# Performance work log

Hardware: AMD Instinct MI355X
Metric: run time of the kernel (lower is better)

The kernel has to match this reference:

```python
import jax, jax.numpy as jnp
import numpy as np

H = 4            # num_heads (forced: 128 projection / d_k=32)
DK = 32          # hardcoded d_k
SCALE = 1.0 / np.sqrt(32.0)
EPS = 1e-5       # LayerNorm eps (torch default)


def setup_inputs() -> dict:
    key = jax.random.key(0)
    ks = jax.random.split(key, 8)
    B, L, Dq, Dkv, M = 16, 4096, 512, 512, 512
    def w(k, shape, fan_in):
        return (jax.random.normal(k, shape, jnp.float32) / np.sqrt(fan_in)).astype(jnp.float32)
    return {
        "Q_in":  jax.random.normal(ks[0], (B, L, Dq),  jnp.float32),
        "KV_in": jax.random.normal(ks[1], (B, L, Dkv), jnp.float32),
        "Wq":  w(ks[2], (Dq, 128), Dq),   "bq":  jnp.zeros((128,), jnp.float32),
        "Wk":  w(ks[3], (Dkv, 128), Dkv), "bk":  jnp.zeros((128,), jnp.float32),
        "Wv":  w(ks[4], (Dkv, 128), Dkv), "bv":  jnp.zeros((128,), jnp.float32),
        "Wo":  w(ks[5], (128, M), 128),   "bo":  jnp.zeros((M,), jnp.float32),
        "Wqo": w(ks[6], (128, M), 128),   "bqo": jnp.zeros((M,), jnp.float32),
        "gamma": jnp.ones((M,), jnp.float32),
        "beta":  jnp.zeros((M,), jnp.float32),
    }


def reference(Q_in, KV_in, Wq, bq, Wk, bk, Wv, bv, Wo, bo, Wqo, bqo, gamma, beta):
    B, L, _ = Q_in.shape
    Qm = Q_in @ Wq + bq          # (B, L, 128)
    Km = KV_in @ Wk + bk         # (B, L, 128)
    Vm = KV_in @ Wv + bv         # (B, L, 128)

    def heads(X):
        # view(B, L, H, DK).permute(0, 2, 3, 1) -> (B, H, DK, L)
        return X.reshape(B, L, H, DK).transpose(0, 2, 3, 1)

    Qh, Kh, Vh = heads(Qm), heads(Km), heads(Vm)
    # matmul contracts over the SEQUENCE dim -> feature-feature scores (B,H,DK,DK)
    scores = jnp.einsum('bhdl,bhel->bhde', Qh, Kh) * SCALE
    attn = jax.nn.softmax(scores, axis=-1)          # dropout = identity (eval)
    out_h = jnp.einsum('bhde,bhel->bhdl', attn, Vh)  # (B, H, DK, L)
    out_h = out_h.transpose(0, 3, 1, 2).reshape(B, L, H * DK)  # (B, L, 128)

    out = out_h @ Wo + bo        # (B, L, M)
    Qm_ = Qm @ Wqo + bqo         # (B, L, M)
    x = Qm_ + out
    mu = jnp.mean(x, axis=-1, keepdims=True)
    var = jnp.var(x, axis=-1, keepdims=True)
    y = (x - mu) * jax.lax.rsqrt(var + EPS) * gamma + beta
    return (y, attn)
```

## Files before the change

### kernel.cpp

```cpp
#include <hip/hip_runtime.h>
#include <hip/hip_bf16.h>

typedef __bf16   bf16x8 __attribute__((ext_vector_type(8)));
typedef _Float16 f16x8  __attribute__((ext_vector_type(8)));
typedef float    f32x4  __attribute__((ext_vector_type(4)));

#define SCALE_QK 0.17677669529663687f
#define LDSS 40
#define TL   136

__device__ __forceinline__ float b2f(ushort u) {
    __hip_bfloat16 h; *reinterpret_cast<ushort*>(&h) = u; return __bfloat162float(h);
}
__device__ __forceinline__ ushort f2b(float f) {
    __hip_bfloat16 h = __float2bfloat16(f); return *reinterpret_cast<ushort*>(&h);
}
__device__ __forceinline__ ushort f2h(float f) {
    union { _Float16 h; ushort u; } x; x.h = (_Float16)f; return x.u;
}
__device__ __forceinline__ uint4 cvt8(float4 a, float4 b) {
    union { uint4 v; ushort u[8]; } H;
    H.u[0] = f2h(a.x); H.u[1] = f2h(a.y); H.u[2] = f2h(a.z); H.u[3] = f2h(a.w);
    H.u[4] = f2h(b.x); H.u[5] = f2h(b.y); H.u[6] = f2h(b.z); H.u[7] = f2h(b.w);
    return H.v;
}

__global__ void k_prep(const float* __restrict__ Wq, const float* __restrict__ Wk,
                       const float* __restrict__ Wv, const float* __restrict__ Wqo,
                       const float* __restrict__ Wo,
                       ushort* __restrict__ WqT, ushort* __restrict__ WkT,
                       ushort* __restrict__ WvT, ushort* __restrict__ WqoT,
                       ushort* __restrict__ WoB) {
    int idx = blockIdx.x * 256 + threadIdx.x;
    int mat = idx >> 16, i = idx & 65535;
    if (mat == 0) {
        int n = i >> 9, k = i & 511;
        WqT[i] = f2h(Wq[k * 128 + n]);
    } else if (mat == 1) {
        int n = i >> 9, k = i & 511;
        WkT[i] = f2h(Wk[k * 128 + n]);
    } else if (mat == 2) {
        int n = i >> 9, k = i & 511;
        WvT[i] = f2h(Wv[k * 128 + n]);
    } else if (mat == 3) {
        int n = i >> 7, k = i & 127;
        WqoT[i] = f2b(Wqo[k * 512 + n]);
    } else if (mat == 4) {
        WoB[i] = f2b(Wo[i]);
    }
}

__global__ __launch_bounds__(256) void k_qkv_scores(
        const float* __restrict__ Qin, const float* __restrict__ KVin,
        const ushort* __restrict__ WqT, const ushort* __restrict__ WkT,
        const ushort* __restrict__ WvT,
        const float* __restrict__ bq, const float* __restrict__ bk,
        const float* __restrict__ bv,
        ushort* __restrict__ QmB, ushort* __restrict__ VmB,
        float* __restrict__ partial) {
    __shared__ __align__(16) ushort lds[2 * 128 * TL];
    ushort* P1  = lds;
    ushort* P2  = lds + 128 * TL;
    ushort* As  = P2;
    ushort* Bs0 = P2 + 128 * LDSS;
    ushort* Bs1 = P2 + 2 * 128 * LDSS;

    const int row0 = blockIdx.x * 128;
    const int tid  = threadIdx.x;
    const int wid  = tid >> 6, lane = tid & 63;
    const int wm = wid >> 1, wn = wid & 1;
    const int quad = lane >> 4, l16 = lane & 15;
    const int sr = tid >> 2;
    const int sc = (tid & 3) * 8;

    float4 aR0, aR1, aR2, aR3;
    uint4  bR0, bR1;
    uint4  cR0, cR1;

    {
        f32x4 acc[4][4] = {};
        {
            const float* Ab = Qin + (size_t)(row0 + sr) * 512 + sc;
            aR0 = *(const float4*)Ab;
            aR1 = *(const float4*)(Ab + 4);
            aR2 = *(const float4*)(Ab + (size_t)64 * 512);
            aR3 = *(const float4*)(Ab + (size_t)64 * 512 + 4);
            bR0 = *(const uint4*)&WqT[(size_t)sr * 512 + sc];
            bR1 = *(const uint4*)&WqT[(size_t)(sr + 64) * 512 + sc];
        }
        for (int k0 = 0; k0 < 512; k0 += 32) {
            __syncthreads();
            *(uint4*)&As[sr * LDSS + sc]        = cvt8(aR0, aR1);
            *(uint4*)&As[(sr + 64) * LDSS + sc] = cvt8(aR2, aR3);
            *(uint4*)&Bs0[sr * LDSS + sc]        = bR0;
            *(uint4*)&Bs0[(sr + 64) * LDSS + sc] = bR1;
            if (k0 < 480) {
                const float* Ab = Qin + (size_t)(row0 + sr) * 512 + k0 + 32 + sc;
                aR0 = *(const float4*)Ab;
                aR1 = *(const float4*)(Ab + 4);
                aR2 = *(const float4*)(Ab + (size_t)64 * 512);
                aR3 = *(const float4*)(Ab + (size_t)64 * 512 + 4);
                bR0 = *(const uint4*)&WqT[(size_t)sr * 512 + k0 + 32 + sc];
                bR1 = *(const uint4*)&WqT[(size_t)(sr + 64) * 512 + k0 + 32 + sc];
            }
            __syncthreads();
            f16x8 aF[4];
#pragma unroll
            for (int i = 0; i < 4; ++i)
                aF[i] = *reinterpret_cast<const f16x8*>(&As[(wm * 64 + i * 16 + l16) * LDSS + quad * 8]);
#pragma unroll
            for (int j = 0; j < 4; ++j) {
                f16x8 bF = *reinterpret_cast<const f16x8*>(&Bs0[(wn * 64 + j * 16 + l16) * LDSS + quad * 8]);
#pragma unroll
                for (int i = 0; i < 4; ++i)
                    acc[i][j] = __builtin_amdgcn_mfma_f32_16x16x32_f16(aF[i], bF, acc[i][j], 0, 0, 0);
            }
        }
        {
            const float* Ab = KVin + (size_t)(row0 + sr) * 512 + sc;
            aR0 = *(const float4*)Ab;
            aR1 = *(const float4*)(Ab + 4);
            aR2 = *(const float4*)(Ab + (size_t)64 * 512);
            aR3 = *(const float4*)(Ab + (size_t)64 * 512 + 4);
            bR0 = *(const uint4*)&WkT[(size_t)sr * 512 + sc];
            bR1 = *(const uint4*)&WkT[(size_t)(sr + 64) * 512 + sc];
            cR0 = *(const uint4*)&WvT[(size_t)sr * 512 + sc];
            cR1 = *(const uint4*)&WvT[(size_t)(sr + 64) * 512 + sc];
        }
#pragma unroll
        for (int j = 0; j < 4; ++j) {
            int col = wn * 64 + j * 16 + l16;
            float bqv = bq[col];
#pragma unroll
            for (int i = 0; i < 4; ++i)
#pragma unroll
                for (int r = 0; r < 4; ++r) {
                    int row = wm * 64 + i * 16 + quad * 4 + r;
                    float v = acc[i][j][r] + bqv;
                    QmB[(size_t)(row0 + row) * 128 + col] = f2b(v);
                    P1[col * TL + row] = f2h(v);
                }
        }
    }

    {
        f32x4 accK[4][4] = {};
        f32x4 accV[4][4] = {};
        for (int k0 = 0; k0 < 512; k0 += 32) {
            __syncthreads();
            *(uint4*)&As[sr * LDSS + sc]        = cvt8(aR0, aR1);
            *(uint4*)&As[(sr + 64) * LDSS + sc] = cvt8(aR2, aR3);
            *(uint4*)&Bs0[sr * LDSS + sc]        = bR0;
            *(uint4*)&Bs0[(sr + 64) * LDSS + sc] = bR1;
            *(uint4*)&Bs1[sr * LDSS + sc]        = cR0;
            *(uint4*)&Bs1[(sr + 64) * LDSS + sc] = cR1;
            if (k0 < 480) {
                const float* Ab = KVin + (size_t)(row0 + sr) * 512 + k0 + 32 + sc;
                aR0 = *(const float4*)Ab;
                aR1 = *(const float4*)(Ab + 4);
                aR2 = *(const float4*)(Ab + (size_t)64 * 512);
                aR3 = *(const float4*)(Ab + (size_t)64 * 512 + 4);
                bR0 = *(const uint4*)&WkT[(size_t)sr * 512 + k0 + 32 + sc];
                bR1 = *(const uint4*)&WkT[(size_t)(sr + 64) * 512 + k0 + 32 + sc];
                cR0 = *(const uint4*)&WvT[(size_t)sr * 512 + k0 + 32 + sc];
                cR1 = *(const uint4*)&WvT[(size_t)(sr + 64) * 512 + k0 + 32 + sc];
            }
            __syncthreads();
            f16x8 aF[4];
#pragma unroll
            for (int i = 0; i < 4; ++i)
                aF[i] = *reinterpret_cast<const f16x8*>(&As[(wm * 64 + i * 16 + l16) * LDSS + quad * 8]);
#pragma unroll
            for (int j = 0; j < 4; ++j) {
                f16x8 bK = *reinterpret_cast<const f16x8*>(&Bs0[(wn * 64 + j * 16 + l16) * LDSS + quad * 8]);
                f16x8 bV = *reinterpret_cast<const f16x8*>(&Bs1[(wn * 64 + j * 16 + l16) * LDSS + quad * 8]);
#pragma unroll
                for (int i = 0; i < 4; ++i) {
                    accK[i][j] = __builtin_amdgcn_mfma_f32_16x16x32_f16(aF[i], bK, accK[i][j], 0, 0, 0);
                    accV[i][j] = __builtin_amdgcn_mfma_f32_16x16x32_f16(aF[i], bV, accV[i][j], 0, 0, 0);
                }
            }
        }
        __syncthreads();
#pragma unroll
        for (int j = 0; j < 4; ++j) {
            int col = wn * 64 + j * 16 + l16;
            float bkv = bk[col], bvv = bv[col];
#pragma unroll
            for (int i = 0; i < 4; ++i)
#pragma unroll
                for (int r = 0; r < 4; ++r) {
                    int row = wm * 64 + i * 16 + quad * 4 + r;
                    float vv = accV[i][j][r] + bvv;
                    VmB[(size_t)(row0 + row) * 128 + col] = f2b(vv);
                    P2[col * TL + row] = f2h(accK[i][j][r] + bkv);
                }
        }
    }
    __syncthreads();

    {
        const int h = wid;
        f32x4 s[2][2] = {};
#pragma unroll
        for (int ks = 0; ks < 4; ++ks) {
            f16x8 qa[2], kb[2];
#pragma unroll
            for (int dt = 0; dt < 2; ++dt)
                qa[dt] = *reinterpret_cast<const f16x8*>(
                    &P1[(h * 32 + dt * 16 + l16) * TL + ks * 32 + quad * 8]);
#pragma unroll
            for (int et = 0; et < 2; ++et)
                kb[et] = *reinterpret_cast<const f16x8*>(
                    &P2[(h * 32 + et * 16 + l16) * TL + ks * 32 + quad * 8]);
#pragma unroll
            for (int dt = 0; dt < 2; ++dt)
#pragma unroll
                for (int et = 0; et < 2; ++et)
                    s[dt][et] = __builtin_amdgcn_mfma_f32_16x16x32_f16(qa[dt], kb[et], s[dt][et], 0, 0, 0);
        }
        const int b = blockIdx.x >> 5, sp = blockIdx.x & 31;
        float* P = partial + (size_t)(sp * 64 + b * 4 + h) * 1024;
#pragma unroll
        for (int dt = 0; dt < 2; ++dt)
#pragma unroll
            for (int et = 0; et < 2; ++et)
#pragma unroll
                for (int r = 0; r < 4; ++r) {
                    int d = dt * 16 + quad * 4 + r, e = et * 16 + l16;
                    P[d * 32 + e] = s[dt][et][r];
                }
    }
}

__global__ __launch_bounds__(256) void k_attn(
        const float* __restrict__ partial, const ushort* __restrict__ WoB,
        float* __restrict__ attnOut, ushort* __restrict__ WcT) {
    int bh = blockIdx.x; int b = bh >> 2, h = bh & 3;
    __shared__ float aS[1024];
    __shared__ __align__(16) ushort wS[32 * 512];
    int t = threadIdx.x;
    for (int i = t; i < 1024; i += 256) {
        float s = 0.f;
#pragma unroll
        for (int sp = 0; sp < 32; ++sp)
            s += partial[(size_t)(sp * 64 + bh) * 1024 + i];
        aS[i] = s * SCALE_QK;
    }
    for (int i = t; i < 2048; i += 256) {
        int r = i >> 6, c = (i & 63) * 8;
        *(uint4*)&wS[r * 512 + c] = *(const uint4*)&WoB[(size_t)(h * 32 + r) * 512 + c];
    }
    __syncthreads();
    if (t < 32) {
        float m = -1e30f;
#pragma unroll
        for (int e = 0; e < 32; ++e) m = fmaxf(m, aS[t * 32 + e]);
        float p[32]; float sum = 0.f;
#pragma unroll
        for (int e = 0; e < 32; ++e) { p[e] = __expf(aS[t * 32 + e] - m); sum += p[e]; }
        float inv = 1.f / sum;
#pragma unroll
        for (int e = 0; e < 32; ++e) aS[t * 32 + e] = p[e] * inv;
    }
    __syncthreads();
    for (int i = t; i < 1024; i += 256)
        attnOut[(size_t)bh * 1024 + i] = aS[i];
    int e = t & 31, mg = t >> 5;
    for (int mi = 0; mi < 64; ++mi) {
        int m = mg * 64 + mi;
        float acc = 0.f;
#pragma unroll
        for (int d = 0; d < 32; ++d)
            acc += aS[d * 32 + e] * b2f(wS[d * 512 + m]);
        WcT[((size_t)b * 512 + m) * 128 + h * 32 + e] = f2b(acc);
    }
}

__global__ __launch_bounds__(256) void k_out_ln(
        const ushort* __restrict__ Vm, const ushort* __restrict__ Qm,
        const ushort* __restrict__ WcT, const ushort* __restrict__ WqoT,
        const float* __restrict__ bo, const float* __restrict__ bqo,
        const float* __restrict__ gamma, const float* __restrict__ beta,
        float* __restrict__ Y) {
    __shared__ __align__(16) ushort As[64 * LDSS];
    __shared__ __align__(16) ushort Bs[512 * LDSS];
    __shared__ float sumS[4][64], sumSS[4][64], muA[64], rsA[64];
    const int row0 = blockIdx.x * 64;
    const int b = row0 >> 12;
    const ushort* WcTb = WcT + (size_t)b * 512 * 128;
    const int tid = threadIdx.x;
    const int wid = tid >> 6, lane = tid & 63;
    const int quad = lane >> 4, l16 = lane & 15;
    const int sr = tid >> 2;
    const int sc = (tid & 3) * 8;

    f32x4 acc[4][8] = {};
    uint4 aR; uint4 bR[8];

    auto issueOL = [&](int k0) {
        const ushort* Asrc; const ushort* Bsrc; int kk;
        if (k0 < 128) { Asrc = Vm; Bsrc = WcTb; kk = k0; }
        else          { Asrc = Qm; Bsrc = WqoT; kk = k0 - 128; }
        aR = *(const uint4*)&Asrc[(size_t)(row0 + sr) * 128 + kk + sc];
#pragma unroll
        for (int p = 0; p < 8; ++p)
            bR[p] = *(const uint4*)&Bsrc[(size_t)(sr + p * 64) * 128 + kk + sc];
    };

    issueOL(0);
    for (int k0 = 0; k0 < 256; k0 += 32) {
        __syncthreads();
        *(uint4*)&As[sr * LDSS + sc] = aR;
#pragma unroll
        for (int p = 0; p < 8; ++p)
            *(uint4*)&Bs[(sr + p * 64) * LDSS + sc] = bR[p];
        if (k0 < 224) issueOL(k0 + 32);
        __syncthreads();
        bf16x8 aF[4];
#pragma unroll
        for (int i = 0; i < 4; ++i)
            aF[i] = *reinterpret_cast<const bf16x8*>(&As[(i * 16 + l16) * LDSS + quad * 8]);
#pragma unroll
        for (int j = 0; j < 8; ++j) {
            bf16x8 bF = *reinterpret_cast<const bf16x8*>(
                &Bs[(wid * 128 + j * 16 + l16) * LDSS + quad * 8]);
#pragma unroll
            for (int i = 0; i < 4; ++i)
                acc[i][j] = __builtin_amdgcn_mfma_f32_16x16x32_bf16(aF[i], bF, acc[i][j], 0, 0, 0);
        }
    }

    float bv[8];
#pragma unroll
    for (int j = 0; j < 8; ++j) {
        int ncol = wid * 128 + j * 16 + l16;
        bv[j] = bo[ncol] + bqo[ncol];
    }
    float sArr[4][4], ssArr[4][4];
#pragma unroll
    for (int i = 0; i < 4; ++i)
#pragma unroll
        for (int r = 0; r < 4; ++r) {
            float s = 0.f, ss = 0.f;
#pragma unroll
            for (int j = 0; j < 8; ++j) {
                float x = acc[i][j][r] + bv[j];
                s += x; ss += x * x;
            }
            sArr[i][r] = s; ssArr[i][r] = ss;
        }
#pragma unroll
    for (int off = 1; off < 16; off <<= 1)
#pragma unroll
        for (int i = 0; i < 4; ++i)
#pragma unroll
            for (int r = 0; r < 4; ++r) {
                sArr[i][r]  += __shfl_xor(sArr[i][r],  off, 64);
                ssArr[i][r] += __shfl_xor(ssArr[i][r], off, 64);
            }
    if (l16 == 0) {
#pragma unroll
        for (int i = 0; i < 4; ++i)
#pragma unroll
            for (int r = 0; r < 4; ++r) {
                int row = i * 16 + quad * 4 + r;
                sumS[wid][row]  = sArr[i][r];
                sumSS[wid][row] = ssArr[i][r];
            }
    }
    __syncthreads();
    if (tid < 64) {
        float s = sumS[0][tid] + sumS[1][tid] + sumS[2][tid] + sumS[3][tid];
        float ss = sumSS[0][tid] + sumSS[1][tid] + sumSS[2][tid] + sumSS[3][tid];
        float mu = s * (1.f / 512.f);
        float var = ss * (1.f / 512.f) - mu * mu;
        muA[tid] = mu;
        rsA[tid] = rsqrtf(var + 1e-5f);
    }
    __syncthreads();

    float gj[8], bj[8];
#pragma unroll
    for (int j = 0; j < 8; ++j) {
        int ncol = wid * 128 + j * 16 + l16;
        gj[j] = gamma[ncol]; bj[j] = beta[ncol];
    }
#pragma unroll
    for (int i = 0; i < 4; ++i)
#pragma unroll
        for (int r = 0; r < 4; ++r) {
            int row = i * 16 + quad * 4 + r;
            float mu = muA[row], rstd = rsA[row];
            size_t base = (size_t)(row0 + row) * 512 + wid * 128 + l16;
#pragma unroll
            for (int j = 0; j < 8; ++j) {
                float x = acc[i][j][r] + bv[j];
                Y[base + j * 16] = (x - mu) * rstd * gj[j] + bj[j];
            }
        }
}

extern "C" void kernel_launch(void* const* d_in, const int* in_sizes, int n_in,
                              void* d_out, int out_size, void* d_ws, size_t ws_size,
                              hipStream_t stream) {
    const float* Qin   = (const float*)d_in[0];
    const float* KVin  = (const float*)d_in[1];
    const float* Wq    = (const float*)d_in[2];
    const float* bq    = (const float*)d_in[3];
    const float* Wk    = (const float*)d_in[4];
    const float* bk    = (const float*)d_in[5];
    const float* Wv    = (const float*)d_in[6];
    const float* bv    = (const float*)d_in[7];
    const float* Wo    = (const float*)d_in[8];
    const float* bo    = (const float*)d_in[9];
    const float* Wqo   = (const float*)d_in[10];
    const float* bqo   = (const float*)d_in[11];
    const float* gamma = (const float*)d_in[12];
    const float* beta  = (const float*)d_in[13];
    float* out = (float*)d_out;
    float* attnOut = out + 33554432;

    char* ws = (char*)d_ws;
    ushort* WqT  = (ushort*)(ws);
    ushort* WkT  = (ushort*)(ws + 131072);
    ushort* WvT  = (ushort*)(ws + 262144);
    ushort* WqoT = (ushort*)(ws + 393216);
    ushort* WoB  = (ushort*)(ws + 524288);
    ushort* QmB  = (ushort*)(ws + 655360);
    ushort* VmB  = (ushort*)(ws + 17432576);
    float*  part = (float*) (ws + 34209792);
    ushort* WcT  = (ushort*)(ws + 42598400);

    k_prep<<<1280, 256, 0, stream>>>(Wq, Wk, Wv, Wqo, Wo,
                                     WqT, WkT, WvT, WqoT, WoB);
    k_qkv_scores<<<512, 256, 0, stream>>>(Qin, KVin, WqT, WkT, WvT,
                                          bq, bk, bv, QmB, VmB, part);
    k_attn<<<64, 256, 0, stream>>>(part, WoB, attnOut, WcT);
    k_out_ln<<<1024, 256, 0, stream>>>(VmB, QmB, WcT, WqoT, bo, bqo, gamma, beta, out);
}
```

Baseline: 472.6 us.

## Split QKV projection from score computation, parallelize k_attn across M tiles

The fused QKV+scores kernel is split in two. The projection kernel now writes fp16 Qm and Km to global memory and uses a smaller LDS footprint, and a new k_scores2 kernel reloads those tiles into swizzled LDS to compute the per-head feature-feature partial scores. k_attn is spread over a 2D grid of four M-quarters, uses a shuffle-based parallel softmax, and keeps Wo in fp32 LDS with the attention column held in registers. Register prefetching is removed from k_out_ln. The aim is higher occupancy and parallelism, paid for with extra global traffic for QmH/KmH, an extra launch, and redundant softmax work across the M-quarters.

```diff
diff --git a/kernel.cpp b/kernel.cpp
--- a/kernel.cpp
+++ b/kernel.cpp
@@ -7,7 +7,7 @@
 
 #define SCALE_QK 0.17677669529663687f
 #define LDSS 40
-#define TL   136
+#define RS   136
 
 __device__ __forceinline__ float b2f(ushort u) {
     __hip_bfloat16 h; *reinterpret_cast<ushort*>(&h) = u; return __bfloat162float(h);
@@ -50,20 +50,17 @@
     }
 }
 
-__global__ __launch_bounds__(256) void k_qkv_scores(
+__global__ __launch_bounds__(256) void k_qkv(
         const float* __restrict__ Qin, const float* __restrict__ KVin,
         const ushort* __restrict__ WqT, const ushort* __restrict__ WkT,
         const ushort* __restrict__ WvT,
         const float* __restrict__ bq, const float* __restrict__ bk,
         const float* __restrict__ bv,
-        ushort* __restrict__ QmB, ushort* __restrict__ VmB,
-        float* __restrict__ partial) {
-    __shared__ __align__(16) ushort lds[2 * 128 * TL];
-    ushort* P1  = lds;
-    ushort* P2  = lds + 128 * TL;
-    ushort* As  = P2;
-    ushort* Bs0 = P2 + 128 * LDSS;
-    ushort* Bs1 = P2 + 2 * 128 * LDSS;
+        ushort* __restrict__ QmB, ushort* __restrict__ QmH,
+        ushort* __restrict__ KmH, ushort* __restrict__ VmB) {
+    __shared__ __align__(16) ushort As [128 * LDSS];
+    __shared__ __align__(16) ushort Bs0[128 * LDSS];
+    __shared__ __align__(16) ushort Bs1[128 * LDSS];
 
     const int row0 = blockIdx.x * 128;
     const int tid  = threadIdx.x;
@@ -138,7 +135,7 @@
                     int row = wm * 64 + i * 16 + quad * 4 + r;
                     float v = acc[i][j][r] + bqv;
                     QmB[(size_t)(row0 + row) * 128 + col] = f2b(v);
-                    P1[col * TL + row] = f2h(v);
+                    QmH[(size_t)(row0 + row) * 128 + col] = f2h(v);
                 }
         }
     }
@@ -181,7 +178,6 @@
                 }
             }
         }
-        __syncthreads();
 #pragma unroll
         for (int j = 0; j < 4; ++j) {
             int col = wn * 64 + j * 16 + l16;
@@ -191,54 +187,77 @@
 #pragma unroll
                 for (int r = 0; r < 4; ++r) {
                     int row = wm * 64 + i * 16 + quad * 4 + r;
-                    float vv = accV[i][j][r] + bvv;
-                    VmB[(size_t)(row0 + row) * 128 + col] = f2b(vv);
-                    P2[col * TL + row] = f2h(accK[i][j][r] + bkv);
+                    KmH[(size_t)(row0 + row) * 128 + col] = f2h(accK[i][j][r] + bkv);
+                    VmB[(size_t)(row0 + row) * 128 + col] = f2b(accV[i][j][r] + bvv);
                 }
         }
     }
+}
+
+__global__ __launch_bounds__(256) void k_scores2(
+        const ushort* __restrict__ QmH, const ushort* __restrict__ KmH,
+        float* __restrict__ partial) {
+    __shared__ __align__(16) ushort Qs[128 * RS];
+    __shared__ __align__(16) ushort Ks[128 * RS];
+    const int bs = blockIdx.x;
+    const int b = bs >> 5, sp = bs & 31;
+    const int t = threadIdx.x;
+    const int wid = t >> 6, lane = t & 63;
+    const int quad = lane >> 4, l16 = lane & 15;
+    const size_t base = ((size_t)b * 4096 + sp * 128) * 128;
+
+#pragma unroll
+    for (int it = 0; it < 8; ++it) {
+        int idx = it * 256 + t;
+        int row = idx >> 4, c8 = (idx & 15) * 8;
+        int swc = c8 ^ (((row >> 3) & 3) << 3);
+        *(uint4*)&Qs[row * RS + swc] = *(const uint4*)&QmH[base + (size_t)row * 128 + c8];
+        *(uint4*)&Ks[row * RS + swc] = *(const uint4*)&KmH[base + (size_t)row * 128 + c8];
+    }
     __syncthreads();
 
-    {
-        const int h = wid;
-        f32x4 s[2][2] = {};
-#pragma unroll
-        for (int ks = 0; ks < 4; ++ks) {
-            f16x8 qa[2], kb[2];
-#pragma unroll
-            for (int dt = 0; dt < 2; ++dt)
-                qa[dt] = *reinterpret_cast<const f16x8*>(
-                    &P1[(h * 32 + dt * 16 + l16) * TL + ks * 32 + quad * 8]);
+    const int h = wid;
+    f32x4 s[2][2] = {};
+#pragma unroll
+    for (int ks = 0; ks < 4; ++ks) {
+        f16x8 qa[2], kb[2];
+#pragma unroll
+        for (int dt = 0; dt < 2; ++dt) {
+            union { f16x8 v; ushort u[8]; } Q, K;
+#pragma unroll
+            for (int z = 0; z < 8; ++z) {
+                int row = ks * 32 + quad * 8 + z;
+                int col = (h * 32 + dt * 16 + l16) ^ (((row >> 3) & 3) << 3);
+                Q.u[z] = Qs[row * RS + col];
+                K.u[z] = Ks[row * RS + col];
+            }
+            qa[dt] = Q.v; kb[dt] = K.v;
+        }
+#pragma unroll
+        for (int dt = 0; dt < 2; ++dt)
 #pragma unroll
             for (int et = 0; et < 2; ++et)
-                kb[et] = *reinterpret_cast<const f16x8*>(
-                    &P2[(h * 32 + et * 16 + l16) * TL + ks * 32 + quad * 8]);
-#pragma unroll
-            for (int dt = 0; dt < 2; ++dt)
-#pragma unroll
-                for (int et = 0; et < 2; ++et)
-                    s[dt][et] = __builtin_amdgcn_mfma_f32_16x16x32_f16(qa[dt], kb[et], s[dt][et], 0, 0, 0);
-        }
-        const int b = blockIdx.x >> 5, sp = blockIdx.x & 31;
-        float* P = partial + (size_t)(sp * 64 + b * 4 + h) * 1024;
-#pragma unroll
-        for (int dt = 0; dt < 2; ++dt)
-#pragma unroll
-            for (int et = 0; et < 2; ++et)
-#pragma unroll
-                for (int r = 0; r < 4; ++r) {
-                    int d = dt * 16 + quad * 4 + r, e = et * 16 + l16;
-                    P[d * 32 + e] = s[dt][et][r];
-                }
-    }
+                s[dt][et] = __builtin_amdgcn_mfma_f32_16x16x32_f16(qa[dt], kb[et], s[dt][et], 0, 0, 0);
+    }
+    float* P = partial + (size_t)(sp * 64 + b * 4 + h) * 1024;
+#pragma unroll
+    for (int dt = 0; dt < 2; ++dt)
+#pragma unroll
+        for (int et = 0; et < 2; ++et)
+#pragma unroll
+            for (int r = 0; r < 4; ++r) {
+                int d = dt * 16 + quad * 4 + r, e = et * 16 + l16;
+                P[d * 32 + e] = s[dt][et][r];
+            }
 }
 
 __global__ __launch_bounds__(256) void k_attn(
         const float* __restrict__ partial, const ushort* __restrict__ WoB,
         float* __restrict__ attnOut, ushort* __restrict__ WcT) {
     int bh = blockIdx.x; int b = bh >> 2, h = bh & 3;
+    int mq = blockIdx.y;
     __shared__ float aS[1024];
-    __shared__ __align__(16) ushort wS[32 * 512];
+    __shared__ float wSf[32 * 128];
     int t = threadIdx.x;
     for (int i = t; i < 1024; i += 256) {
         float s = 0.f;
@@ -247,32 +266,46 @@
             s += partial[(size_t)(sp * 64 + bh) * 1024 + i];
         aS[i] = s * SCALE_QK;
     }
-    for (int i = t; i < 2048; i += 256) {
-        int r = i >> 6, c = (i & 63) * 8;
-        *(uint4*)&wS[r * 512 + c] = *(const uint4*)&WoB[(size_t)(h * 32 + r) * 512 + c];
+    for (int i = t; i < 4096; i += 256) {
+        int r = i >> 7, c = i & 127;
+        wSf[i] = b2f(WoB[(size_t)(h * 32 + r) * 512 + mq * 128 + c]);
     }
     __syncthreads();
-    if (t < 32) {
-        float m = -1e30f;
-#pragma unroll
-        for (int e = 0; e < 32; ++e) m = fmaxf(m, aS[t * 32 + e]);
-        float p[32]; float sum = 0.f;
-#pragma unroll
-        for (int e = 0; e < 32; ++e) { p[e] = __expf(aS[t * 32 + e] - m); sum += p[e]; }
-        float inv = 1.f / sum;
-#pragma unroll
-        for (int e = 0; e < 32; ++e) aS[t * 32 + e] = p[e] * inv;
+    {
+        int row = t >> 3, sub = t & 7;
+        float v[4];
+#pragma unroll
+        for (int z = 0; z < 4; ++z) v[z] = aS[row * 32 + sub * 4 + z];
+        float m = fmaxf(fmaxf(v[0], v[1]), fmaxf(v[2], v[3]));
+#pragma unroll
+        for (int off = 1; off < 8; off <<= 1)
+            m = fmaxf(m, __shfl_xor(m, off, 64));
+        float pz[4], s = 0.f;
+#pragma unroll
+        for (int z = 0; z < 4; ++z) { pz[z] = __expf(v[z] - m); s += pz[z]; }
+#pragma unroll
+        for (int off = 1; off < 8; off <<= 1)
+            s += __shfl_xor(s, off, 64);
+        float inv = 1.f / s;
+#pragma unroll
+        for (int z = 0; z < 4; ++z) aS[row * 32 + sub * 4 + z] = pz[z] * inv;
     }
     __syncthreads();
-    for (int i = t; i < 1024; i += 256)
-        attnOut[(size_t)bh * 1024 + i] = aS[i];
+    if (mq == 0)
+        for (int i = t; i < 1024; i += 256)
+            attnOut[(size_t)bh * 1024 + i] = aS[i];
     int e = t & 31, mg = t >> 5;
-    for (int mi = 0; mi < 64; ++mi) {
-        int m = mg * 64 + mi;
+    float prow[32];
+#pragma unroll
+    for (int d = 0; d < 32; ++d) prow[d] = aS[d * 32 + e];
+#pragma unroll 4
+    for (int mi = 0; mi < 16; ++mi) {
+        int ml = mg * 16 + mi;
         float acc = 0.f;
 #pragma unroll
         for (int d = 0; d < 32; ++d)
-            acc += aS[d * 32 + e] * b2f(wS[d * 512 + m]);
+            acc += prow[d] * wSf[d * 128 + ml];
+        int m = mq * 128 + ml;
         WcT[((size_t)b * 512 + m) * 128 + h * 32 + e] = f2b(acc);
     }
 }
@@ -296,26 +329,19 @@
     const int sc = (tid & 3) * 8;
 
     f32x4 acc[4][8] = {};
-    uint4 aR; uint4 bR[8];
-
-    auto issueOL = [&](int k0) {
+
+    for (int k0 = 0; k0 < 256; k0 += 32) {
         const ushort* Asrc; const ushort* Bsrc; int kk;
         if (k0 < 128) { Asrc = Vm; Bsrc = WcTb; kk = k0; }
         else          { Asrc = Qm; Bsrc = WqoT; kk = k0 - 128; }
-        aR = *(const uint4*)&Asrc[(size_t)(row0 + sr) * 128 + kk + sc];
-#pragma unroll
-        for (int p = 0; p < 8; ++p)
-            bR[p] = *(const uint4*)&Bsrc[(size_t)(sr + p * 64) * 128 + kk + sc];
-    };
-
-    issueOL(0);
-    for (int k0 = 0; k0 < 256; k0 += 32) {
         __syncthreads();
-        *(uint4*)&As[sr * LDSS + sc] = aR;
-#pragma unroll
-        for (int p = 0; p < 8; ++p)
-            *(uint4*)&Bs[(sr + p * 64) * LDSS + sc] = bR[p];
-        if (k0 < 224) issueOL(k0 + 32);
+        *(uint4*)&As[sr * LDSS + sc] =
+            *(const uint4*)&Asrc[(size_t)(row0 + sr) * 128 + kk + sc];
+#pragma unroll
+        for (int p = 0; p < 8; ++p) {
+            int r = sr + p * 64;
+            *(uint4*)&Bs[r * LDSS + sc] = *(const uint4*)&Bsrc[(size_t)r * 128 + kk + sc];
+        }
         __syncthreads();
         bf16x8 aF[4];
 #pragma unroll
@@ -428,14 +454,17 @@
     ushort* WqoT = (ushort*)(ws + 393216);
     ushort* WoB  = (ushort*)(ws + 524288);
     ushort* QmB  = (ushort*)(ws + 655360);
-    ushort* VmB  = (ushort*)(ws + 17432576);
-    float*  part = (float*) (ws + 34209792);
-    ushort* WcT  = (ushort*)(ws + 42598400);
+    ushort* QmH  = (ushort*)(ws + 17432576);
+    ushort* KmH  = (ushort*)(ws + 34209792);
+    ushort* VmB  = (ushort*)(ws + 50987008);
+    float*  part = (float*) (ws + 67764224);
+    ushort* WcT  = (ushort*)(ws + 76152832);
 
     k_prep<<<1280, 256, 0, stream>>>(Wq, Wk, Wv, Wqo, Wo,
                                      WqT, WkT, WvT, WqoT, WoB);
-    k_qkv_scores<<<512, 256, 0, stream>>>(Qin, KVin, WqT, WkT, WvT,
-                                          bq, bk, bv, QmB, VmB, part);
-    k_attn<<<64, 256, 0, stream>>>(part, WoB, attnOut, WcT);
+    k_qkv<<<512, 256, 0, stream>>>(Qin, KVin, WqT, WkT, WvT,
+                                   bq, bk, bv, QmB, QmH, KmH, VmB);
+    k_scores2<<<512, 256, 0, stream>>>(QmH, KmH, part);
+    k_attn<<<dim3(64, 4), 256, 0, stream>>>(part, WoB, attnOut, WcT);
     k_out_ln<<<1024, 256, 0, stream>>>(VmB, QmB, WcT, WqoT, bo, bqo, gamma, beta, out);
 }
```

After: 436.5 us. -7.6%, faster.

## Switch intermediates to fp16, split k_attn over output columns, parallelize softmax

Applied to the files above, without the earlier changes.

Stores Qm, Vm, Wo, Wqo and the combined Wc intermediates as fp16 instead of bf16 and uses the f16 MFMA in the output/LayerNorm kernel. This lets the Q projection write one converted value to both global memory and LDS. k_attn now launches a 4x wider grid split over output columns, so 256 blocks share the Wo-combination work instead of 64. It also computes the softmax with all 256 threads using shuffles rather than 32 threads. The register prefetch in k_out_ln is removed, trading load/compute overlap for lower register pressure, and fp16 has a narrower dynamic range than bf16.

```diff
diff --git a/kernel.cpp b/kernel.cpp
--- a/kernel.cpp
+++ b/kernel.cpp
@@ -17,6 +17,9 @@
 }
 __device__ __forceinline__ ushort f2h(float f) {
     union { _Float16 h; ushort u; } x; x.h = (_Float16)f; return x.u;
+}
+__device__ __forceinline__ float h2f(ushort u) {
+    union { _Float16 h; ushort u; } x; x.u = u; return (float)x.h;
 }
 __device__ __forceinline__ uint4 cvt8(float4 a, float4 b) {
     union { uint4 v; ushort u[8]; } H;
@@ -30,7 +33,7 @@
                        const float* __restrict__ Wo,
                        ushort* __restrict__ WqT, ushort* __restrict__ WkT,
                        ushort* __restrict__ WvT, ushort* __restrict__ WqoT,
-                       ushort* __restrict__ WoB) {
+                       ushort* __restrict__ WoH) {
     int idx = blockIdx.x * 256 + threadIdx.x;
     int mat = idx >> 16, i = idx & 65535;
     if (mat == 0) {
@@ -44,9 +47,9 @@
         WvT[i] = f2h(Wv[k * 128 + n]);
     } else if (mat == 3) {
         int n = i >> 7, k = i & 127;
-        WqoT[i] = f2b(Wqo[k * 512 + n]);
+        WqoT[i] = f2h(Wqo[k * 512 + n]);
     } else if (mat == 4) {
-        WoB[i] = f2b(Wo[i]);
+        WoH[i] = f2h(Wo[i]);
     }
 }
 
@@ -56,7 +59,7 @@
         const ushort* __restrict__ WvT,
         const float* __restrict__ bq, const float* __restrict__ bk,
         const float* __restrict__ bv,
-        ushort* __restrict__ QmB, ushort* __restrict__ VmB,
+        ushort* __restrict__ QmH, ushort* __restrict__ VmH,
         float* __restrict__ partial) {
     __shared__ __align__(16) ushort lds[2 * 128 * TL];
     ushort* P1  = lds;
@@ -137,8 +140,9 @@
                 for (int r = 0; r < 4; ++r) {
                     int row = wm * 64 + i * 16 + quad * 4 + r;
                     float v = acc[i][j][r] + bqv;
-                    QmB[(size_t)(row0 + row) * 128 + col] = f2b(v);
-                    P1[col * TL + row] = f2h(v);
+                    ushort hv = f2h(v);
+                    QmH[(size_t)(row0 + row) * 128 + col] = hv;
+                    P1[col * TL + row] = hv;
                 }
         }
     }
@@ -191,8 +195,7 @@
 #pragma unroll
                 for (int r = 0; r < 4; ++r) {
                     int row = wm * 64 + i * 16 + quad * 4 + r;
-                    float vv = accV[i][j][r] + bvv;
-                    VmB[(size_t)(row0 + row) * 128 + col] = f2b(vv);
+                    VmH[(size_t)(row0 + row) * 128 + col] = f2h(accV[i][j][r] + bvv);
                     P2[col * TL + row] = f2h(accK[i][j][r] + bkv);
                 }
         }
@@ -234,11 +237,12 @@
 }
 
 __global__ __launch_bounds__(256) void k_attn(
-        const float* __restrict__ partial, const ushort* __restrict__ WoB,
+        const float* __restrict__ partial, const ushort* __restrict__ WoH,
         float* __restrict__ attnOut, ushort* __restrict__ WcT) {
     int bh = blockIdx.x; int b = bh >> 2, h = bh & 3;
+    int mq = blockIdx.y;
     __shared__ float aS[1024];
-    __shared__ __align__(16) ushort wS[32 * 512];
+    __shared__ float wSf[32 * 128];
     int t = threadIdx.x;
     for (int i = t; i < 1024; i += 256) {
         float s = 0.f;
@@ -247,33 +251,47 @@
             s += partial[(size_t)(sp * 64 + bh) * 1024 + i];
         aS[i] = s * SCALE_QK;
     }
-    for (int i = t; i < 2048; i += 256) {
-        int r = i >> 6, c = (i & 63) * 8;
-        *(uint4*)&wS[r * 512 + c] = *(const uint4*)&WoB[(size_t)(h * 32 + r) * 512 + c];
+    for (int i = t; i < 4096; i += 256) {
+        int r = i >> 7, c = i & 127;
+        wSf[i] = h2f(WoH[(size_t)(h * 32 + r) * 512 + mq * 128 + c]);
     }
     __syncthreads();
-    if (t < 32) {
-        float m = -1e30f;
-#pragma unroll
-        for (int e = 0; e < 32; ++e) m = fmaxf(m, aS[t * 32 + e]);
-        float p[32]; float sum = 0.f;
-#pragma unroll
-        for (int e = 0; e < 32; ++e) { p[e] = __expf(aS[t * 32 + e] - m); sum += p[e]; }
-        float inv = 1.f / sum;
-#pragma unroll
-        for (int e = 0; e < 32; ++e) aS[t * 32 + e] = p[e] * inv;
+    {
+        int row = t >> 3, sub = t & 7;
+        float v[4];
+#pragma unroll
+        for (int z = 0; z < 4; ++z) v[z] = aS[row * 32 + sub * 4 + z];
+        float m = fmaxf(fmaxf(v[0], v[1]), fmaxf(v[2], v[3]));
+#pragma unroll
+        for (int off = 1; off < 8; off <<= 1)
+            m = fmaxf(m, __shfl_xor(m, off, 64));
+        float pz[4], s = 0.f;
+#pragma unroll
+        for (int z = 0; z < 4; ++z) { pz[z] = __expf(v[z] - m); s += pz[z]; }
+#pragma unroll
+        for (int off = 1; off < 8; off <<= 1)
+            s += __shfl_xor(s, off, 64);
+        float inv = 1.f / s;
+#pragma unroll
+        for (int z = 0; z < 4; ++z) aS[row * 32 + sub * 4 + z] = pz[z] * inv;
     }
     __syncthreads();
-    for (int i = t; i < 1024; i += 256)
-        attnOut[(size_t)bh * 1024 + i] = aS[i];
+    if (mq == 0)
+        for (int i = t; i < 1024; i += 256)
+            attnOut[(size_t)bh * 1024 + i] = aS[i];
     int e = t & 31, mg = t >> 5;
-    for (int mi = 0; mi < 64; ++mi) {
-        int m = mg * 64 + mi;
+    float prow[32];
+#pragma unroll
+    for (int d = 0; d < 32; ++d) prow[d] = aS[d * 32 + e];
+#pragma unroll 4
+    for (int mi = 0; mi < 16; ++mi) {
+        int ml = mg * 16 + mi;
         float acc = 0.f;
 #pragma unroll
         for (int d = 0; d < 32; ++d)
-            acc += aS[d * 32 + e] * b2f(wS[d * 512 + m]);
-        WcT[((size_t)b * 512 + m) * 128 + h * 32 + e] = f2b(acc);
+            acc += prow[d] * wSf[d * 128 + ml];
+        int m = mq * 128 + ml;
+        WcT[((size_t)b * 512 + m) * 128 + h * 32 + e] = f2h(acc);
     }
 }
 
@@ -296,38 +314,31 @@
     const int sc = (tid & 3) * 8;
 
     f32x4 acc[4][8] = {};
-    uint4 aR; uint4 bR[8];
-
-    auto issueOL = [&](int k0) {
+
+    for (int k0 = 0; k0 < 256; k0 += 32) {
         const ushort* Asrc; const ushort* Bsrc; int kk;
         if (k0 < 128) { Asrc = Vm; Bsrc = WcTb; kk = k0; }
         else          { Asrc = Qm; Bsrc = WqoT; kk = k0 - 128; }
-        aR = *(const uint4*)&Asrc[(size_t)(row0 + sr) * 128 + kk + sc];
-#pragma unroll
-        for (int p = 0; p < 8; ++p)
-            bR[p] = *(const uint4*)&Bsrc[(size_t)(sr + p * 64) * 128 + kk + sc];
-    };
-
-    issueOL(0);
-    for (int k0 = 0; k0 < 256; k0 += 32) {
         __syncthreads();
-        *(uint4*)&As[sr * LDSS + sc] = aR;
-#pragma unroll
-        for (int p = 0; p < 8; ++p)
-            *(uint4*)&Bs[(sr + p * 64) * LDSS + sc] = bR[p];
-        if (k0 < 224) issueOL(k0 + 32);
+        *(uint4*)&As[sr * LDSS + sc] =
+            *(const uint4*)&Asrc[(size_t)(row0 + sr) * 128 + kk + sc];
+#pragma unroll
+        for (int p = 0; p < 8; ++p) {
+            int r = sr + p * 64;
+            *(uint4*)&Bs[r * LDSS + sc] = *(const uint4*)&Bsrc[(size_t)r * 128 + kk + sc];
+        }
         __syncthreads();
-        bf16x8 aF[4];
+        f16x8 aF[4];
 #pragma unroll
         for (int i = 0; i < 4; ++i)
-            aF[i] = *reinterpret_cast<const bf16x8*>(&As[(i * 16 + l16) * LDSS + quad * 8]);
+            aF[i] = *reinterpret_cast<const f16x8*>(&As[(i * 16 + l16) * LDSS + quad * 8]);
 #pragma unroll
         for (int j = 0; j < 8; ++j) {
-            bf16x8 bF = *reinterpret_cast<const bf16x8*>(
+            f16x8 bF = *reinterpret_cast<const f16x8*>(
                 &Bs[(wid * 128 + j * 16 + l16) * LDSS + quad * 8]);
 #pragma unroll
             for (int i = 0; i < 4; ++i)
-                acc[i][j] = __builtin_amdgcn_mfma_f32_16x16x32_bf16(aF[i], bF, acc[i][j], 0, 0, 0);
+                acc[i][j] = __builtin_amdgcn_mfma_f32_16x16x32_f16(aF[i], bF, acc[i][j], 0, 0, 0);
         }
     }
 
@@ -426,16 +437,16 @@
     ushort* WkT  = (ushort*)(ws + 131072);
     ushort* WvT  = (ushort*)(ws + 262144);
     ushort* WqoT = (ushort*)(ws + 393216);
-    ushort* WoB  = (ushort*)(ws + 524288);
-    ushort* QmB  = (ushort*)(ws + 655360);
-    ushort* VmB  = (ushort*)(ws + 17432576);
+    ushort* WoH  = (ushort*)(ws + 524288);
+    ushort* QmH  = (ushort*)(ws + 655360);
+    ushort* VmH  = (ushort*)(ws + 17432576);
     float*  part = (float*) (ws + 34209792);
     ushort* WcT  = (ushort*)(ws + 42598400);
 
     k_prep<<<1280, 256, 0, stream>>>(Wq, Wk, Wv, Wqo, Wo,
-                                     WqT, WkT, WvT, WqoT, WoB);
+                                     WqT, WkT, WvT, WqoT, WoH);
     k_qkv_scores<<<512, 256, 0, stream>>>(Qin, KVin, WqT, WkT, WvT,
-                                          bq, bk, bv, QmB, VmB, part);
-    k_attn<<<64, 256, 0, stream>>>(part, WoB, attnOut, WcT);
-    k_out_ln<<<1024, 256, 0, stream>>>(VmB, QmB, WcT, WqoT, bo, bqo, gamma, beta, out);
-}
+                                          bq, bk, bv, QmH, VmH, part);
+    k_attn<<<dim3(64, 4), 256, 0, stream>>>(part, WoH, attnOut, WcT);
+    k_out_ln<<<1024, 256, 0, stream>>>(VmH, QmH, WcT, WqoT, bo, bqo, gamma, beta, out);
+}
```

New measurement: 419.5 us. 1.13x faster.
